# Kernel optimization log

Measured on AMD Instinct MI355X. Metric: run time of the kernel, lower is better.

The kernel has to match this reference:

```python
import jax, jax.numpy as jnp
import numpy as np

EPS = 1e-5
K = 9
DILATION = 1

def bn(x, g, b, m, v):
    # x: (B,C,N,1), inference-mode BatchNorm2d with running stats
    sh = (1, -1, 1, 1)
    return (x - m.reshape(sh)) * (g.reshape(sh) / jnp.sqrt(v.reshape(sh) + EPS)) + b.reshape(sh)

def conv1x1(x, w, b):
    # w: (Cout, Cin), x: (B,Cin,N,1)
    return jnp.einsum('oc,bcnj->bonj', w, x) + b.reshape(1, -1, 1, 1)

def knn_idx(feat, k):
    # feat: (B,C,N) -> (B,N,k) indices of k nearest nodes (incl. self)
    xt = jnp.transpose(feat, (0, 2, 1))  # (B,N,C)
    x2 = jnp.sum(xt * xt, axis=-1)       # (B,N)
    dist = x2[:, :, None] - 2.0 * jnp.einsum('bnc,bmc->bnm', xt, xt) + x2[:, None, :]
    _, idx = jax.lax.top_k(-dist, k)
    return idx

def setup_inputs():
    key = jax.random.key(0)
    ks = jax.random.split(key, 24)
    B, C, H, W = 16, 256, 32, 32
    HID = 512
    def g(i, shape, s=1.0):
        return jax.random.normal(ks[i], shape, dtype=jnp.float32) * s
    def pos(i, shape):
        return jax.random.uniform(ks[i], shape, dtype=jnp.float32, minval=0.5, maxval=1.5)
    return {
        'x': g(0, (B, C, H, W)),
        'fc1_w': g(1, (C, C), 0.05), 'fc1_b': g(2, (C,), 0.05),
        'bn1_g': pos(3, (C,)), 'bn1_b': g(4, (C,), 0.1), 'bn1_m': g(5, (C,), 0.1), 'bn1_v': pos(6, (C,)),
        'gc_w': g(7, (HID, 2 * C), 0.05), 'gc_b': g(8, (HID,), 0.05),
        'gbn_g': pos(9, (HID,)), 'gbn_b': g(10, (HID,), 0.1), 'gbn_m': g(11, (HID,), 0.1), 'gbn_v': pos(12, (HID,)),
        'bn2_g': pos(13, (HID,)), 'bn2_b': g(14, (HID,), 0.1), 'bn2_m': g(15, (HID,), 0.1), 'bn2_v': pos(16, (HID,)),
        'fc2_w': g(17, (C, HID), 0.05), 'fc2_b': g(18, (C,), 0.05),
        'bn3_g': pos(19, (C,)), 'bn3_b': g(20, (C,), 0.1), 'bn3_m': g(21, (C,), 0.1), 'bn3_v': pos(22, (C,)),
    }

def reference(x, fc1_w, fc1_b, bn1_g, bn1_b, bn1_m, bn1_v,
              gc_w, gc_b, gbn_g, gbn_b, gbn_m, gbn_v,
              bn2_g, bn2_b, bn2_m, bn2_v,
              fc2_w, fc2_b, bn3_g, bn3_b, bn3_m, bn3_v):
    B, C, H, W = x.shape
    N = H * W
    x = x.reshape(B, C, N, 1)
    shortcut = x
    # fc1: 1x1 conv + BN
    h = bn(conv1x1(x, fc1_w, fc1_b), bn1_g, bn1_b, bn1_m, bn1_v)
    # DyGraphConv2d: dynamic dilated kNN graph over N nodes
    feat = h[..., 0]  # (B,C,N)
    idx = knn_idx(feat, K * DILATION)[:, :, ::DILATION]  # (B,N,K)
    # MRConv2d: max over neighbors of (x_j - x_i)
    x_j = jax.vmap(lambda f, i: f[:, i])(feat, idx)        # (B,C,N,K) gather
    diff_max = jnp.max(x_j - feat[:, :, :, None], axis=-1)  # (B,C,N)
    # interleave [x, max_diff] along channel dim -> (B, 2C, N, 1)
    m = jnp.stack([feat, diff_max], axis=2).reshape(B, 2 * C, N, 1)
    g = conv1x1(m, gc_w, gc_b)
    g = bn(g, gbn_g, gbn_b, gbn_m, gbn_v)  # BasicConv BN, act='None'
    # graph_conv Sequential: BN + GELU (erf, torch default)
    g = jax.nn.gelu(bn(g, bn2_g, bn2_b, bn2_m, bn2_v), approximate=False)
    # fc2 + residual (drop_path=0 -> identity)
    out = bn(conv1x1(g, fc2_w, fc2_b), bn3_g, bn3_b, bn3_m, bn3_v)
    return out + shortcut
```

## Files before the change

kernel.cpp:

```cpp
#include <hip/hip_runtime.h>
#include <hip/hip_bf16.h>
#include <stdint.h>

typedef unsigned long long u64;
typedef __hip_bfloat16 bf16;
typedef short s8v __attribute__((ext_vector_type(8)));
typedef short s4v __attribute__((ext_vector_type(4)));
typedef float f4v __attribute__((ext_vector_type(4)));

#define B_   16
#define C_   256
#define N_   1024
#define HID_ 512

#define GLD16(g, l)                                                         \
    __builtin_amdgcn_global_load_lds(                                       \
        (const __attribute__((address_space(1))) void*)(g),                 \
        (__attribute__((address_space(3))) void*)(l), 16, 0, 0)

__device__ __forceinline__ unsigned short f2b(float f) {
    unsigned u = __float_as_uint(f);
    unsigned r = (u + 0x7FFFu + ((u >> 16) & 1u)) >> 16;
    return (unsigned short)r;
}
__device__ __forceinline__ float b2f(unsigned short s) {
    return __uint_as_float(((unsigned)s) << 16);
}
__device__ __forceinline__ float ldIn(const void* p, long long i, int bf) {
    return bf ? b2f(((const unsigned short*)p)[i]) : ((const float*)p)[i];
}
__device__ __forceinline__ u64 shfl_xor_u64(u64 v, int m) {
    unsigned lo = (unsigned)v, hi = (unsigned)(v >> 32);
    lo = __shfl_xor(lo, m, 64);
    hi = __shfl_xor(hi, m, 64);
    return ((u64)hi << 32) | lo;
}

__global__ void prep_kernel(const void* xp,
    const void* fc1_b, const void* bn1_g, const void* bn1_b, const void* bn1_m, const void* bn1_v,
    const void* gc_b,  const void* gbn_g, const void* gbn_b, const void* gbn_m, const void* gbn_v,
    const void* bn2_g, const void* bn2_b, const void* bn2_m, const void* bn2_v,
    const void* fc2_b, const void* bn3_g, const void* bn3_b, const void* bn3_m, const void* bn3_v,
    int* flags, float* s1, float* t1, float* Sg, float* Tg, float* s3, float* t3,
    float* x2)
{
    __shared__ int sf;
    if (threadIdx.x == 0) {
        const unsigned short* u = (const unsigned short*)xp;
        int cnt = 0;
        for (int i = 0; i < 64; ++i) {
            int e = (u[2 * i] >> 7) & 0xFF;
            cnt += (e >= 87 && e <= 167);
        }
        int f = (cnt >= 48) ? 1 : 0;
        flags[0] = f;
        sf = f;
    }
    for (int i = threadIdx.x; i < B_ * N_; i += 512) x2[i] = 0.f;
    __syncthreads();
    int bf = sf;
    int i = threadIdx.x;
    if (i < 256) {
        float g = ldIn(bn1_g, i, bf), bb = ldIn(bn1_b, i, bf);
        float m = ldIn(bn1_m, i, bf), v  = ldIn(bn1_v, i, bf);
        float s = g / sqrtf(v + 1e-5f);
        s1[i] = s;
        t1[i] = (ldIn(fc1_b, i, bf) - m) * s + bb;

        float g3 = ldIn(bn3_g, i, bf), b3 = ldIn(bn3_b, i, bf);
        float m3 = ldIn(bn3_m, i, bf), v3 = ldIn(bn3_v, i, bf);
        float ss3 = g3 / sqrtf(v3 + 1e-5f);
        s3[i] = ss3;
        t3[i] = (ldIn(fc2_b, i, bf) - m3) * ss3 + b3;
    }
    if (i < 512) {
        float gg = ldIn(gbn_g, i, bf), gb = ldIn(gbn_b, i, bf);
        float gm = ldIn(gbn_m, i, bf), gv = ldIn(gbn_v, i, bf);
        float sg = gg / sqrtf(gv + 1e-5f);
        float g2 = ldIn(bn2_g, i, bf), b2 = ldIn(bn2_b, i, bf);
        float m2 = ldIn(bn2_m, i, bf), v2 = ldIn(bn2_v, i, bf);
        float s2 = g2 / sqrtf(v2 + 1e-5f);
        Sg[i] = sg * s2;
        Tg[i] = ((ldIn(gc_b, i, bf) - gm) * sg + gb - m2) * s2 + b2;
    }
}

__global__ __launch_bounds__(256)
void cast_weights(const void* w1, const void* wg, const void* w2,
                  short* W1h, short* W1l, short* Wgb, short* W2b,
                  const int* flags)
{
    int inf = flags[0];
    int i = blockIdx.x * 256 + threadIdx.x;
    if (i < 65536) {
        float f = ldIn(w1, i, inf);
        unsigned short h = f2b(f);
        W1h[i] = (short)h;
        W1l[i] = (short)f2b(f - b2f(h));
    } else if (i < 65536 + 262144) {
        int j = i - 65536;
        Wgb[j] = (short)f2b(ldIn(wg, j, inf));
    } else {
        int j = i - 327680;
        W2b[j] = (short)f2b(ldIn(w2, j, inf));
    }
}

__global__ __launch_bounds__(256)
void transpose_split_x(const void* __restrict__ X, short* __restrict__ xth,
                       short* __restrict__ xtl, const int* __restrict__ flags)
{
    __shared__ float tile[64][68];
    int inf = flags[0];
    int t = threadIdx.x;
    int n0 = blockIdx.x * 64, c0 = blockIdx.y * 64, b = blockIdx.z;

    #pragma unroll
    for (int rr = 0; rr < 4; ++rr) {
        int cl = (t >> 4) + rr * 16;
        int nl = (t & 15) * 4;
        long long g = ((long long)b * C_ + c0 + cl) * N_ + n0 + nl;
        if (inf) {
            s4v v = *(const s4v*)((const short*)X + g);
            tile[cl][nl + 0] = b2f((unsigned short)v[0]);
            tile[cl][nl + 1] = b2f((unsigned short)v[1]);
            tile[cl][nl + 2] = b2f((unsigned short)v[2]);
            tile[cl][nl + 3] = b2f((unsigned short)v[3]);
        } else {
            f4v v = *(const f4v*)((const float*)X + g);
            tile[cl][nl + 0] = v[0]; tile[cl][nl + 1] = v[1];
            tile[cl][nl + 2] = v[2]; tile[cl][nl + 3] = v[3];
        }
    }
    __syncthreads();

    int nl = t >> 2, cseg = t & 3;
    long long base = ((long long)((b << 10) + n0 + nl)) * C_ + c0 + cseg * 16;
    s8v h0, h1, l0, l1;
    #pragma unroll
    for (int cc = 0; cc < 16; ++cc) {
        float f = tile[cseg * 16 + cc][nl];
        unsigned short h = f2b(f);
        unsigned short l = f2b(f - b2f(h));
        if (cc < 8) { h0[cc] = (short)h; l0[cc] = (short)l; }
        else        { h1[cc - 8] = (short)h; l1[cc - 8] = (short)l; }
    }
    *(s8v*)(xth + base)     = h0;
    *(s8v*)(xth + base + 8) = h1;
    *(s8v*)(xtl + base)     = l0;
    *(s8v*)(xtl + base + 8) = l1;
}

__global__ __launch_bounds__(256)
void fc1_mfma(const short* __restrict__ W1h, const short* __restrict__ W1l,
              const short* __restrict__ xth, const short* __restrict__ xtl,
              const float* __restrict__ s1, const float* __restrict__ t1,
              float* __restrict__ Ft, short* __restrict__ Fhi,
              short* __restrict__ Flo, float* __restrict__ x2)
{
    __shared__ __align__(16) char ldsbuf[32768];

    int t = threadIdx.x;
    int n0 = blockIdx.x * 64, o0 = blockIdx.y * 128, b = blockIdx.z;
    int wv = t >> 6, lane = t & 63, ln15 = t & 15, quad = (t >> 4) & 3;

    int csw = (((lane & 3) ^ ((lane >> 3) & 3))) * 8;
    const short* gAh = W1h + (long long)(o0 + wv * 32 + (lane >> 2)) * C_ + csw;
    const short* gAl = W1l + (long long)(o0 + wv * 32 + (lane >> 2)) * C_ + csw;
    short* lH0 = (short*)(ldsbuf)           + wv * 32 * 32;
    short* lL0 = (short*)(ldsbuf + 8192)    + wv * 32 * 32;
    short* lH1 = (short*)(ldsbuf + 16384)   + wv * 32 * 32;
    short* lL1 = (short*)(ldsbuf + 24576)   + wv * 32 * 32;

#define FC1_STAGE(kc_, bi_) do {                                              \
        short* dh = (bi_) ? lH1 : lH0;                                        \
        short* dl = (bi_) ? lL1 : lL0;                                        \
        GLD16(gAh + (kc_) * 32,            dh);                               \
        GLD16(gAh + (kc_) * 32 + 16 * C_,  dh + 16 * 32);                     \
        GLD16(gAl + (kc_) * 32,            dl);                               \
        GLD16(gAl + (kc_) * 32 + 16 * C_,  dl + 16 * 32);                     \
    } while (0)

    FC1_STAGE(0, 0);

    s8v xh[8], xl[8];
    {
        long long xoff = (long long)((b << 10) + n0 + wv * 16 + ln15) * C_ + quad * 8;
        #pragma unroll
        for (int kc = 0; kc < 8; ++kc) {
            xh[kc] = *(const s8v*)(xth + xoff + kc * 32);
            xl[kc] = *(const s8v*)(xtl + xoff + kc * 32);
        }
    }

    f4v acc[8];
    #pragma unroll
    for (int i = 0; i < 8; ++i) acc[i] = 0.f;

    int roff = (quad ^ ((ln15 >> 1) & 3)) * 8;

    __syncthreads();

    #pragma unroll
    for (int kc = 0; kc < 8; ++kc) {
        if (kc < 7) FC1_STAGE(kc + 1, (kc + 1) & 1);
        const short* Ah_c = (const short*)(ldsbuf + (kc & 1) * 16384);
        const short* Al_c = Ah_c + 4096;
        #pragma unroll
        for (int i = 0; i < 8; ++i) {
            s8v wh8 = *(const s8v*)&Ah_c[(i * 16 + ln15) * 32 + roff];
            s8v wl8 = *(const s8v*)&Al_c[(i * 16 + ln15) * 32 + roff];
            acc[i] = __builtin_amdgcn_mfma_f32_16x16x32_bf16(wh8, xh[kc], acc[i], 0, 0, 0);
            acc[i] = __builtin_amdgcn_mfma_f32_16x16x32_bf16(wh8, xl[kc], acc[i], 0, 0, 0);
            acc[i] = __builtin_amdgcn_mfma_f32_16x16x32_bf16(wl8, xh[kc], acc[i], 0, 0, 0);
        }
        __syncthreads();
    }
#undef FC1_STAGE

    int n = n0 + wv * 16 + ln15;
    long long nb = (long long)(b << 10) + n;
    float p2 = 0.f;
    #pragma unroll
    for (int i = 0; i < 8; ++i) {
        int ob = o0 + i * 16 + quad * 4;
        f4v f;
        s4v hi, lo;
        #pragma unroll
        for (int r = 0; r < 4; ++r) {
            float v = acc[i][r] * s1[ob + r] + t1[ob + r];
            f[r] = v;
            unsigned short h = f2b(v);
            hi[r] = (short)h;
            lo[r] = (short)f2b(v - b2f(h));
            p2 += v * v;
        }
        *(f4v*)(Ft  + nb * C_ + ob) = f;
        *(s4v*)(Fhi + nb * C_ + ob) = hi;
        *(s4v*)(Flo + nb * C_ + ob) = lo;
    }
    p2 += __shfl_xor(p2, 16, 64);
    p2 += __shfl_xor(p2, 32, 64);
    if (quad == 0) atomicAdd(&x2[nb], p2);
}

__global__ __launch_bounds__(256)
void gram_topk(const short* __restrict__ Fhi, const short* __restrict__ Flo,
               const float* __restrict__ x2, u64* __restrict__ Part)
{
    __shared__ __align__(16) char ldsbuf[33280];
    float* x2s = (float*)(ldsbuf + 32768);
    u64*   mrg  = (u64*)(ldsbuf);
    u64*   mrg2 = (u64*)(ldsbuf + 20480);

    int t = threadIdx.x;
    int q0 = blockIdx.x * 64, mq = blockIdx.y, b = blockIdx.z;
    int wv = t >> 6, lane = t & 63, ln15 = t & 15, quad = (t >> 4) & 3;

    int csw = (((lane & 3) ^ ((lane >> 3) & 3))) * 8;
    const short* gAh = Fhi + (long long)((b << 10) + mq * 128 + wv * 32 + (lane >> 2)) * C_ + csw;
    const short* gAl = Flo + (long long)((b << 10) + mq * 128 + wv * 32 + (lane >> 2)) * C_ + csw;
    short* lH0 = (short*)(ldsbuf)           + wv * 32 * 32;
    short* lL0 = (short*)(ldsbuf + 8192)    + wv * 32 * 32;
    short* lH1 = (short*)(ldsbuf + 16384)   + wv * 32 * 32;
    short* lL1 = (short*)(ldsbuf + 24576)   + wv * 32 * 32;

#define GRAM_STAGE(kc_, bi_) do {                                             \
        short* dh = (bi_) ? lH1 : lH0;                                        \
        short* dl = (bi_) ? lL1 : lL0;                                        \
        GLD16(gAh + (kc_) * 32,            dh);                               \
        GLD16(gAh + (kc_) * 32 + 16 * C_,  dh + 16 * 32);                     \
        GLD16(gAl + (kc_) * 32,            dl);                               \
        GLD16(gAl + (kc_) * 32 + 16 * C_,  dl + 16 * 32);                     \
    } while (0)

    GRAM_STAGE(0, 0);

    if (t < 128) x2s[t] = x2[(b << 10) + mq * 128 + t];

    s8v qh[8], ql[8];
    {
        long long qoff = (long long)((b << 10) + q0 + wv * 16 + ln15) * C_ + quad * 8;
        #pragma unroll
        for (int kc = 0; kc < 8; ++kc) {
            qh[kc] = *(const s8v*)(Fhi + qoff + kc * 32);
            ql[kc] = *(const s8v*)(Flo + qoff + kc * 32);
        }
    }

    f4v acc[8];
    #pragma unroll
    for (int i = 0; i < 8; ++i) acc[i] = 0.f;

    int roff = (quad ^ ((ln15 >> 1) & 3)) * 8;

    __syncthreads();

    #pragma unroll
    for (int kc = 0; kc < 8; ++kc) {
        if (kc < 7) GRAM_STAGE(kc + 1, (kc + 1) & 1);
        const short* Ah_c = (const short*)(ldsbuf + (kc & 1) * 16384);
        const short* Al_c = Ah_c + 4096;
        #pragma unroll
        for (int i = 0; i < 8; ++i) {
            s8v mh = *(const s8v*)&Ah_c[(i * 16 + ln15) * 32 + roff];
            s8v ml = *(const s8v*)&Al_c[(i * 16 + ln15) * 32 + roff];
            acc[i] = __builtin_amdgcn_mfma_f32_16x16x32_bf16(mh, qh[kc], acc[i], 0, 0, 0);
            acc[i] = __builtin_amdgcn_mfma_f32_16x16x32_bf16(mh, ql[kc], acc[i], 0, 0, 0);
            acc[i] = __builtin_amdgcn_mfma_f32_16x16x32_bf16(ml, qh[kc], acc[i], 0, 0, 0);
        }
        __syncthreads();
    }
#undef GRAM_STAGE

    u64 l[9];
    #pragma unroll
    for (int i = 0; i < 9; ++i) l[i] = ~0ULL;
    #pragma unroll
    for (int i = 0; i < 8; ++i) {
        #pragma unroll
        for (int r = 0; r < 4; ++r) {
            int mloc = i * 16 + quad * 4 + r;
            float d = x2s[mloc] - 2.f * acc[i][r];
            unsigned u = __float_as_uint(d);
            u = (u & 0x80000000u) ? ~u : (u | 0x80000000u);
            u64 key = ((u64)u << 32) | (unsigned)(mq * 128 + mloc);
            if (key < l[8]) {
                u64 x = key;
                #pragma unroll
                for (int jj = 0; jj < 9; ++jj) {
                    u64 lo2 = l[jj] < x ? l[jj] : x;
                    u64 hi2 = l[jj] < x ? x : l[jj];
                    l[jj] = lo2; x = hi2;
                }
            }
        }
    }

    __syncthreads();
    {
        int qloc = wv * 16 + ln15;
        #pragma unroll
        for (int k = 0; k < 9; ++k) mrg[(qloc * 4 + quad) * 9 + k] = l[k];
    }
    __syncthreads();
    if (t < 128) {
        int r = t >> 1, pr = t & 1;
        const u64* LA = &mrg[(r * 4 + pr * 2) * 9];
        const u64* LB = LA + 9;
        int ia = 0, ib = 0;
        u64* Po = &mrg2[(r * 2 + pr) * 9];
        #pragma unroll
        for (int k = 0; k < 9; ++k) {
            u64 va = LA[ia], vb = LB[ib];
            bool ta = va < vb;
            Po[k] = ta ? va : vb;
            ia += ta; ib += !ta;
        }
    }
    __syncthreads();
    if (t < 64) {
        const u64* LA = &mrg2[(t * 2) * 9];
        const u64* LB = LA + 9;
        int ia = 0, ib = 0;
        u64* P = Part + (((long long)((b << 10) + q0 + t)) * 8 + mq) * 9;
        #pragma unroll
        for (int k = 0; k < 9; ++k) {
            u64 va = LA[ia], vb = LB[ib];
            bool ta = va < vb;
            P[k] = ta ? va : vb;
            ia += ta; ib += !ta;
        }
    }
}

__global__ __launch_bounds__(256)
void build_Mt(const float* __restrict__ Ft, const u64* __restrict__ Part,
              short* __restrict__ Mt)
{
    int t = threadIdx.x;
    int wv = t >> 6, lane = t & 63;
    int n = blockIdx.x * 4 + wv;
    int b = blockIdx.y;
    long long nb = (long long)(b << 10) + n;

    const u64* L = Part + nb * 72 + (long long)(lane & 7) * 9;
    u64 l[9];
    #pragma unroll
    for (int k = 0; k < 9; ++k) l[k] = L[k];
    #pragma unroll
    for (int s = 1; s <= 4; s <<= 1) {
        u64 p[9];
        #pragma unroll
        for (int k = 0; k < 9; ++k) p[k] = shfl_xor_u64(l[k], s);
        #pragma unroll
        for (int k = 0; k < 9; ++k) {
            u64 x = p[k];
            if (x < l[8]) {
                #pragma unroll
                for (int jj = 0; jj < 9; ++jj) {
                    u64 lo2 = l[jj] < x ? l[jj] : x;
                    u64 hi2 = l[jj] < x ? x : l[jj];
                    l[jj] = lo2; x = hi2;
                }
            }
        }
    }

    int c0 = lane * 4;
    f4v f = *(const f4v*)(Ft + nb * C_ + c0);
    f4v mx = {-3.4e38f, -3.4e38f, -3.4e38f, -3.4e38f};
    #pragma unroll
    for (int k = 0; k < 9; ++k) {
        int id = (int)(l[k] & 0xFFFFFFFFu);
        f4v g = *(const f4v*)(Ft + ((long long)(b << 10) + id) * C_ + c0);
        mx[0] = fmaxf(mx[0], g[0]); mx[1] = fmaxf(mx[1], g[1]);
        mx[2] = fmaxf(mx[2], g[2]); mx[3] = fmaxf(mx[3], g[3]);
    }
    s8v m8;
    #pragma unroll
    for (int r = 0; r < 4; ++r) {
        m8[2 * r]     = (short)f2b(f[r]);
        m8[2 * r + 1] = (short)f2b(mx[r] - f[r]);
    }
    *(s8v*)(Mt + nb * (2 * C_) + 2 * c0) = m8;
}

template<int EPI>
__global__ __launch_bounds__(256)
void mfma_gemm(const short* __restrict__ A, const short* __restrict__ Bm,
               void* __restrict__ Out, const float* __restrict__ scale,
               const float* __restrict__ bias, const void* __restrict__ resid,
               const int* __restrict__ flags, int K, int Odim)
{
    __shared__ __align__(16) short As[128 * 40];
    __shared__ __align__(16) short Bs[64 * 40];

    int t = threadIdx.x, b = blockIdx.z;
    int n0 = blockIdx.x * 64, o0 = blockIdx.y * 128;
    int wv = t >> 6, ln15 = t & 15, quad = (t >> 4) & 3;

    f4v acc[8];
    #pragma unroll
    for (int i = 0; i < 8; ++i) acc[i] = 0.f;

    int nkc = K >> 5;
    for (int kc = 0; kc < nkc; ++kc) {
        __syncthreads();
        #pragma unroll
        for (int s = 0; s < 3; ++s) {
            int sid = t + s * 256;
            int row = sid >> 2, seg = sid & 3;
            if (row < 128)
                *(s8v*)&As[row * 40 + seg * 8] =
                    *(const s8v*)(A + (long long)(o0 + row) * K + kc * 32 + seg * 8);
            else
                *(s8v*)&Bs[(row - 128) * 40 + seg * 8] =
                    *(const s8v*)(Bm + ((long long)((b << 10) + n0 + row - 128)) * K + kc * 32 + seg * 8);
        }
        __syncthreads();
        s8v bf = *(s8v*)&Bs[(wv * 16 + ln15) * 40 + quad * 8];
        #pragma unroll
        for (int i = 0; i < 8; ++i) {
            s8v a = *(s8v*)&As[(i * 16 + ln15) * 40 + quad * 8];
            acc[i] = __builtin_amdgcn_mfma_f32_16x16x32_bf16(a, bf, acc[i], 0, 0, 0);
        }
    }

    int inf = flags[0];
    int n = n0 + wv * 16 + ln15;
    #pragma unroll
    for (int i = 0; i < 8; ++i) {
        int ob = o0 + i * 16 + quad * 4;
        if (EPI == 0) {
            s4v g;
            #pragma unroll
            for (int r = 0; r < 4; ++r) {
                float val = acc[i][r] * scale[ob + r] + bias[ob + r];
                val = 0.5f * val * (1.0f + erff(val * 0.70710678118654752f));
                g[r] = (short)f2b(val);
            }
            *(s4v*)((short*)Out + ((long long)((b << 10) + n)) * Odim + ob) = g;
        } else {
            #pragma unroll
            for (int r = 0; r < 4; ++r) {
                int o = ob + r;
                long long oi = ((long long)b * Odim + o) * N_ + n;
                ((float*)Out)[oi] = acc[i][r] * scale[o] + bias[o] + ldIn(resid, oi, inf);
            }
        }
    }
}

extern "C" void kernel_launch(void* const* d_in, const int* in_sizes, int n_in,
                              void* d_out, int out_size, void* d_ws, size_t ws_size,
                              hipStream_t stream)
{
    const void* p[23];
    if (n_in >= 23 && in_sizes[0] != 4194304 && in_sizes[22] == 4194304) {
        const int amap[23] = {
            22, 13, 12, 1, 0, 2, 3,
            21, 20, 17, 16, 18, 19,
            5, 4, 6, 7,
            15, 14, 9, 8, 10, 11 };
        for (int i = 0; i < 23; ++i) p[i] = d_in[amap[i]];
    } else {
        for (int i = 0; i < 23; ++i) p[i] = d_in[i];
    }

    const void* x     = p[0];
    const void* fc1_w = p[1];
    const void* fc1_b = p[2];
    const void* bn1_g = p[3];
    const void* bn1_b = p[4];
    const void* bn1_m = p[5];
    const void* bn1_v = p[6];
    const void* gc_w  = p[7];
    const void* gc_b  = p[8];
    const void* gbn_g = p[9];
    const void* gbn_b = p[10];
    const void* gbn_m = p[11];
    const void* gbn_v = p[12];
    const void* bn2_g = p[13];
    const void* bn2_b = p[14];
    const void* bn2_m = p[15];
    const void* bn2_v = p[16];
    const void* fc2_w = p[17];
    const void* fc2_b = p[18];
    const void* bn3_g = p[19];
    const void* bn3_b = p[20];
    const void* bn3_m = p[21];
    const void* bn3_v = p[22];

    char* ws = (char*)d_ws;
    size_t off = 0;
    int*   flags = (int*)ws;
    float* s1 = (float*)(ws + 256);
    float* t1 = s1 + 256;
    float* s3 = t1 + 256;
    float* t3 = s3 + 256;
    float* Sg = t3 + 256;
    float* Tg = Sg + 512;
    off = 16384;
    short* W1h   = (short*)(ws + off); off += (size_t)C_ * C_ * 2;
    short* W1l   = (short*)(ws + off); off += (size_t)C_ * C_ * 2;
    short* Wgb   = (short*)(ws + off); off += (size_t)HID_ * 2 * C_ * 2;
    short* W2b   = (short*)(ws + off); off += (size_t)C_ * HID_ * 2;
    short* xth   = (short*)(ws + off); off += (size_t)B_ * N_ * C_ * 2;
    short* xtl   = (short*)(ws + off); off += (size_t)B_ * N_ * C_ * 2;
    float* Ft    = (float*)(ws + off); off += (size_t)B_ * N_ * C_ * 4;
    short* Fhi   = (short*)(ws + off); off += (size_t)B_ * N_ * C_ * 2;
    short* Flo   = (short*)(ws + off); off += (size_t)B_ * N_ * C_ * 2;
    float* x2    = (float*)(ws + off); off += (size_t)B_ * N_ * 4;
    u64*   Part  = (u64*)  (ws + off); off += (size_t)B_ * N_ * 8 * 9 * 8;
    short* Mt    = (short*)(ws + off); off += (size_t)B_ * N_ * 2 * C_ * 2;
    short* Gt    = (short*)(ws + off); off += (size_t)B_ * N_ * HID_ * 2;

    prep_kernel<<<1, 512, 0, stream>>>(x,
        fc1_b, bn1_g, bn1_b, bn1_m, bn1_v,
        gc_b, gbn_g, gbn_b, gbn_m, gbn_v,
        bn2_g, bn2_b, bn2_m, bn2_v,
        fc2_b, bn3_g, bn3_b, bn3_m, bn3_v,
        flags, s1, t1, Sg, Tg, s3, t3, x2);

    cast_weights<<<1792, 256, 0, stream>>>(fc1_w, gc_w, fc2_w,
                                           W1h, W1l, Wgb, W2b, flags);

    transpose_split_x<<<dim3(16, 4, 16), 256, 0, stream>>>(x, xth, xtl, flags);

    fc1_mfma<<<dim3(16, 2, 16), 256, 0, stream>>>(
        W1h, W1l, xth, xtl, s1, t1, Ft, Fhi, Flo, x2);

    gram_topk<<<dim3(16, 8, 16), 256, 0, stream>>>(Fhi, Flo, x2, Part);

    build_Mt<<<dim3(256, 16), 256, 0, stream>>>(Ft, Part, Mt);

    mfma_gemm<0><<<dim3(16, 4, 16), 256, 0, stream>>>(
        Wgb, Mt, Gt, Sg, Tg, nullptr, flags, 2 * C_, HID_);

    mfma_gemm<1><<<dim3(16, 2, 16), 256, 0, stream>>>(
        W2b, Gt, d_out, s3, t3, x, flags, HID_, C_);
}
```

Measured before the change: 287.1 us.

## Pipeline GEMM weight tiles via async LDS loads and keep B operand in registers

The generic bf16 GEMM used for the graph conv and fc2 now fixes K at compile time. It keeps each wave's activation fragments in registers for the whole K loop and streams the weight tile through double-buffered LDS using direct global-to-LDS loads with an XOR swizzle, replacing the synchronous copy-then-compute loop. Separately, gram_topk reads the squared norms straight from global memory as vectors instead of staging them in LDS. This should overlap loads with MFMA work and cut LDS traffic and barriers, at the cost of more registers per thread (up to 16 s8v fragments).

```diff
diff --git a/kernel.cpp b/kernel.cpp
--- a/kernel.cpp
+++ b/kernel.cpp
@@ -248,8 +248,7 @@
 void gram_topk(const short* __restrict__ Fhi, const short* __restrict__ Flo,
                const float* __restrict__ x2, u64* __restrict__ Part)
 {
-    __shared__ __align__(16) char ldsbuf[33280];
-    float* x2s = (float*)(ldsbuf + 32768);
+    __shared__ __align__(16) char ldsbuf[32768];
     u64*   mrg  = (u64*)(ldsbuf);
     u64*   mrg2 = (u64*)(ldsbuf + 20480);
 
@@ -276,8 +275,6 @@
 
     GRAM_STAGE(0, 0);
 
-    if (t < 128) x2s[t] = x2[(b << 10) + mq * 128 + t];
-
     s8v qh[8], ql[8];
     {
         long long qoff = (long long)((b << 10) + q0 + wv * 16 + ln15) * C_ + quad * 8;
@@ -313,15 +310,18 @@
     }
 #undef GRAM_STAGE
 
+    const float* x2p = x2 + (b << 10) + mq * 128 + quad * 4;
+
     u64 l[9];
     #pragma unroll
     for (int i = 0; i < 9; ++i) l[i] = ~0ULL;
     #pragma unroll
     for (int i = 0; i < 8; ++i) {
+        f4v xv = *(const f4v*)(x2p + i * 16);
         #pragma unroll
         for (int r = 0; r < 4; ++r) {
             int mloc = i * 16 + quad * 4 + r;
-            float d = x2s[mloc] - 2.f * acc[i][r];
+            float d = xv[r] - 2.f * acc[i][r];
             unsigned u = __float_as_uint(d);
             u = (u & 0x80000000u) ? ~u : (u | 0x80000000u);
             u64 key = ((u64)u << 32) | (unsigned)(mq * 128 + mloc);
@@ -426,46 +426,61 @@
     *(s8v*)(Mt + nb * (2 * C_) + 2 * c0) = m8;
 }
 
-template<int EPI>
+template<int EPI, int K_>
 __global__ __launch_bounds__(256)
 void mfma_gemm(const short* __restrict__ A, const short* __restrict__ Bm,
                void* __restrict__ Out, const float* __restrict__ scale,
                const float* __restrict__ bias, const void* __restrict__ resid,
-               const int* __restrict__ flags, int K, int Odim)
-{
-    __shared__ __align__(16) short As[128 * 40];
-    __shared__ __align__(16) short Bs[64 * 40];
+               const int* __restrict__ flags, int Odim)
+{
+    __shared__ __align__(16) char ldsbuf[16384];
 
     int t = threadIdx.x, b = blockIdx.z;
     int n0 = blockIdx.x * 64, o0 = blockIdx.y * 128;
-    int wv = t >> 6, ln15 = t & 15, quad = (t >> 4) & 3;
+    int wv = t >> 6, lane = t & 63, ln15 = t & 15, quad = (t >> 4) & 3;
+
+    int csw = (((lane & 3) ^ ((lane >> 3) & 3))) * 8;
+    const short* gA = A + (long long)(o0 + wv * 32 + (lane >> 2)) * K_ + csw;
+    short* l0 = (short*)(ldsbuf)        + wv * 32 * 32;
+    short* l1 = (short*)(ldsbuf + 8192) + wv * 32 * 32;
+
+#define GEMM_STAGE(kc_, bi_) do {                                             \
+        short* d = (bi_) ? l1 : l0;                                           \
+        GLD16(gA + (kc_) * 32,            d);                                 \
+        GLD16(gA + (kc_) * 32 + 16 * K_,  d + 16 * 32);                       \
+    } while (0)
+
+    GEMM_STAGE(0, 0);
+
+    constexpr int NKC = K_ / 32;
+    s8v bfr[NKC];
+    {
+        long long boff = (long long)((b << 10) + n0 + wv * 16 + ln15) * K_ + quad * 8;
+        #pragma unroll
+        for (int kc = 0; kc < NKC; ++kc)
+            bfr[kc] = *(const s8v*)(Bm + boff + kc * 32);
+    }
 
     f4v acc[8];
     #pragma unroll
     for (int i = 0; i < 8; ++i) acc[i] = 0.f;
 
-    int nkc = K >> 5;
-    for (int kc = 0; kc < nkc; ++kc) {
+    int roff = (quad ^ ((ln15 >> 1) & 3)) * 8;
+
+    __syncthreads();
+
+    #pragma unroll
+    for (int kc = 0; kc < NKC; ++kc) {
+        if (kc < NKC - 1) GEMM_STAGE(kc + 1, (kc + 1) & 1);
+        const short* Ac = (const short*)(ldsbuf + (kc & 1) * 8192);
+        #pragma unroll
+        for (int i = 0; i < 8; ++i) {
+            s8v a = *(const s8v*)&Ac[(i * 16 + ln15) * 32 + roff];
+            acc[i] = __builtin_amdgcn_mfma_f32_16x16x32_bf16(a, bfr[kc], acc[i], 0, 0, 0);
+        }
         __syncthreads();
-        #pragma unroll
-        for (int s = 0; s < 3; ++s) {
-            int sid = t + s * 256;
-            int row = sid >> 2, seg = sid & 3;
-            if (row < 128)
-                *(s8v*)&As[row * 40 + seg * 8] =
-                    *(const s8v*)(A + (long long)(o0 + row) * K + kc * 32 + seg * 8);
-            else
-                *(s8v*)&Bs[(row - 128) * 40 + seg * 8] =
-                    *(const s8v*)(Bm + ((long long)((b << 10) + n0 + row - 128)) * K + kc * 32 + seg * 8);
-        }
-        __syncthreads();
-        s8v bf = *(s8v*)&Bs[(wv * 16 + ln15) * 40 + quad * 8];
-        #pragma unroll
-        for (int i = 0; i < 8; ++i) {
-            s8v a = *(s8v*)&As[(i * 16 + ln15) * 40 + quad * 8];
-            acc[i] = __builtin_amdgcn_mfma_f32_16x16x32_bf16(a, bf, acc[i], 0, 0, 0);
-        }
-    }
+    }
+#undef GEMM_STAGE
 
     int inf = flags[0];
     int n = n0 + wv * 16 + ln15;
@@ -575,9 +590,9 @@
 
     build_Mt<<<dim3(256, 16), 256, 0, stream>>>(Ft, Part, Mt);
 
-    mfma_gemm<0><<<dim3(16, 4, 16), 256, 0, stream>>>(
-        Wgb, Mt, Gt, Sg, Tg, nullptr, flags, 2 * C_, HID_);
-
-    mfma_gemm<1><<<dim3(16, 2, 16), 256, 0, stream>>>(
-        W2b, Gt, d_out, s3, t3, x, flags, HID_, C_);
-}
+    mfma_gemm<0, 512><<<dim3(16, 4, 16), 256, 0, stream>>>(
+        Wgb, Mt, Gt, Sg, Tg, nullptr, flags, HID_);
+
+    mfma_gemm<1, 512><<<dim3(16, 2, 16), 256, 0, stream>>>(
+        W2b, Gt, d_out, s3, t3, x, flags, C_);
+}
```

Measured after the change: 294.8 us. 2.7% more time.
